# Kernel optimization log

Measured on AMD Instinct MI355X. Metric: run time of the kernel, lower is better.

Reference implementation:

```python
import jax, jax.numpy as jnp
import numpy as np

B, S, EMB, HEAD = 8, 2048, 2048, 128
ROPE_BASE = 10000.0


def _rope(x):
    # x: [B, S, D]; standard rotate-half rotary position embedding
    d = x.shape[-1]
    half = d // 2
    inv_freq = 1.0 / (ROPE_BASE ** (jnp.arange(half, dtype=jnp.float32) / half))  # [half]
    ang = jnp.arange(x.shape[-2], dtype=jnp.float32)[:, None] * inv_freq           # [S, half]
    cos, sin = jnp.cos(ang), jnp.sin(ang)
    x1, x2 = x[..., :half], x[..., half:]
    return jnp.concatenate([x1 * cos - x2 * sin, x1 * sin + x2 * cos], axis=-1)


def setup_inputs() -> dict:
    key = jax.random.key(0)
    ks = jax.random.split(key, 7)
    sc = 1.0 / np.sqrt(EMB)
    return {
        "x": jax.random.normal(ks[0], (B, S, EMB), dtype=jnp.float32),
        "Wq": jax.random.normal(ks[1], (EMB, HEAD), dtype=jnp.float32) * sc,
        "bq": jax.random.normal(ks[2], (HEAD,), dtype=jnp.float32) * 0.02,
        "Wk": jax.random.normal(ks[3], (EMB, HEAD), dtype=jnp.float32) * sc,
        "bk": jax.random.normal(ks[4], (HEAD,), dtype=jnp.float32) * 0.02,
        "Wv": jax.random.normal(ks[5], (EMB, HEAD), dtype=jnp.float32) * sc,
        "bv": jax.random.normal(ks[6], (HEAD,), dtype=jnp.float32) * 0.02,
    }


def reference(x, Wq, bq, Wk, bk, Wv, bv):
    # single-head causal self-attention with RoPE (cache=None path)
    q = _rope(x @ Wq + bq)            # [B, S, HEAD]
    k = _rope(x @ Wk + bk)            # [B, S, HEAD]
    v = x @ Wv + bv                   # [B, S, HEAD]
    scale = 1.0 / jnp.sqrt(jnp.float32(HEAD))
    scores = jnp.einsum('bqd,bkd->bqk', q, k) * scale   # [B, S, S]
    causal = jnp.tril(jnp.ones((S, S), dtype=bool))
    scores = jnp.where(causal, scores, -jnp.inf)
    weights = jax.nn.softmax(scores, axis=-1)
    return jnp.einsum('bqk,bkd->bqd', weights, v)       # [B, S, HEAD]
```

## Files before the change

kernel.cpp:

```cpp
#include <hip/hip_runtime.h>

typedef __bf16 bf16;
typedef __bf16 bf16x8 __attribute__((ext_vector_type(8)));
typedef float f32x4 __attribute__((ext_vector_type(4)));

#define S_LEN 2048
#define EMBD 2048
#define HD 128

__device__ inline void gload16(const void* g, void* l) {
  __builtin_amdgcn_global_load_lds(
      (const __attribute__((address_space(1))) unsigned int*)g,
      (__attribute__((address_space(3))) unsigned int*)l, 16, 0, 0);
}

__global__ void k_prep(const float* __restrict__ Wq, const float* __restrict__ Wk,
                       const float* __restrict__ Wv, bf16* __restrict__ wt) {
  int idx = blockIdx.x * blockDim.x + threadIdx.x;
  int k = idx & 2047;
  int n = (idx >> 11) & 127;
  int mat = idx >> 18;
  int ksrc = (k & ~63) | ((k & 63) ^ ((n & 7) << 3));
  const float* W = (mat == 0) ? Wq : ((mat == 1) ? Wk : Wv);
  wt[idx] = (bf16)W[(size_t)ksrc * HD + n];
}

__global__ __launch_bounds__(256) void k_qkv(
    const float* __restrict__ x, const bf16* __restrict__ wt,
    const float* __restrict__ bq, const float* __restrict__ bk,
    const float* __restrict__ bv, bf16* __restrict__ Qw, bf16* __restrict__ Kw,
    bf16* __restrict__ Vtw) {
  __shared__ __align__(16) bf16 xs[2][64 * 72];
  __shared__ __align__(16) bf16 wts[2][192 * 64];

  const int tid = threadIdx.x;
  const int lane = tid & 63;
  const int wn = tid >> 6;
  const int l15 = lane & 15;
  const int lh = lane >> 4;
  const int bx = blockIdx.x & 255;
  const int by = blockIdx.x >> 8;
  const int row0 = bx * 64;

  f32x4 acc[4][3];
#pragma unroll
  for (int mf = 0; mf < 4; ++mf)
#pragma unroll
    for (int f = 0; f < 3; ++f) acc[mf][f] = {};

  int xr_[4], xk_[4];
  const float* xp_[4];
#pragma unroll
  for (int i = 0; i < 4; ++i) {
    int e = (i * 256 + tid) * 4;
    xr_[i] = e >> 6;
    xk_[i] = e & 63;
    xp_[i] = x + (size_t)(row0 + xr_[i]) * EMBD + xk_[i];
  }

  const bf16* wp[6];
  int we[6];
#pragma unroll
  for (int i = 0; i < 6; ++i) {
    int e = (i * 256 + tid) * 8;
    int np = e >> 6, k = e & 63;
    int ng = (np < 128) ? by * 128 + np : 256 + by * 64 + (np - 128);
    wp[i] = wt + (size_t)ng * EMBD + k;
    we[i] = e;
  }

  auto stage_issue = [&](int ks, int buf, float4* xr) {
#pragma unroll
    for (int i = 0; i < 4; ++i) xr[i] = *(const float4*)(xp_[i] + ks * 64);
#pragma unroll
    for (int i = 0; i < 6; ++i) gload16(wp[i] + ks * 64, &wts[buf][we[i]]);
  };
  auto xwrite = [&](int buf, const float4* xr) {
#pragma unroll
    for (int i = 0; i < 4; ++i) {
      union { bf16 h[4]; uint2 u; } p;
      p.h[0] = (bf16)xr[i].x; p.h[1] = (bf16)xr[i].y;
      p.h[2] = (bf16)xr[i].z; p.h[3] = (bf16)xr[i].w;
      *(uint2*)&xs[buf][xr_[i] * 72 + xk_[i]] = p.u;
    }
  };

  {
    float4 xr[4];
    stage_issue(0, 0, xr);
    xwrite(0, xr);
  }
  __syncthreads();

  for (int ks = 0; ks < EMBD / 64; ++ks) {
    const int c = ks & 1, pbuf = c ^ 1;
    float4 xr[4];
    if (ks < EMBD / 64 - 1) stage_issue(ks + 1, pbuf, xr);

#pragma unroll
    for (int kk = 0; kk < 2; ++kk) {
      bf16x8 a[4];
#pragma unroll
      for (int mf = 0; mf < 4; ++mf)
        a[mf] = *(const bf16x8*)&xs[c][(mf * 16 + l15) * 72 + kk * 32 + lh * 8];
      const int klin = (kk * 32 + lh * 8) ^ ((l15 & 7) << 3);
#pragma unroll
      for (int f = 0; f < 3; ++f) {
        bf16x8 b = *(const bf16x8*)&wts[c][(f * 64 + wn * 16 + l15) * 64 + klin];
#pragma unroll
        for (int mf = 0; mf < 4; ++mf)
          acc[mf][f] =
              __builtin_amdgcn_mfma_f32_16x16x32_bf16(a[mf], b, acc[mf][f], 0, 0, 0);
      }
    }

    if (ks < EMBD / 64 - 1) xwrite(pbuf, xr);
    __syncthreads();
  }

  bf16* vstage = wts[0];

  {
    const int colA = by * 128 + wn * 16 + l15;
    const int colB = colA + 64;
    float biasA = (colA < 128) ? bq[colA] : bk[colA - 128];
    float biasB = (colB < 128) ? bq[colB] : bk[colB - 128];
    float invf = exp2f((float)(colA & 63) * -0.20762050593046014f);
#pragma unroll
    for (int mf = 0; mf < 4; ++mf) {
#pragma unroll
      for (int r = 0; r < 4; ++r) {
        int grow = row0 + mf * 16 + lh * 4 + r;
        int s = grow & (S_LEN - 1);
        int bb = grow >> 11;
        float xa = acc[mf][0][r] + biasA;
        float xb = acc[mf][1][r] + biasB;
        float sn, cs;
        sincosf((float)s * invf, &sn, &cs);
        float oa = xa * cs - xb * sn;
        float ob = xa * sn + xb * cs;
        if (by == 0) {
          Qw[(size_t)(bb * S_LEN + s) * HD + colA] = (bf16)oa;
          Qw[(size_t)(bb * S_LEN + s) * HD + colB] = (bf16)ob;
        } else {
          int ccA = colA - 128, ccB = colB - 128;
          int sw = (s & 7) << 3;
          Kw[(size_t)(bb * S_LEN + s) * HD + (ccA ^ sw)] = (bf16)oa;
          Kw[(size_t)(bb * S_LEN + s) * HD + (ccB ^ sw)] = (bf16)ob;
        }
      }
    }
  }
  {
    const int dvl = wn * 16 + l15;
    float biasV = bv[by * 64 + dvl];
#pragma unroll
    for (int mf = 0; mf < 4; ++mf)
#pragma unroll
      for (int r = 0; r < 4; ++r) {
        int mrow = mf * 16 + lh * 4 + r;
        vstage[dvl * 72 + mrow] = (bf16)(acc[mf][2][r] + biasV);
      }
  }
  __syncthreads();
  {
    int bb = row0 >> 11;
    int s0 = row0 & (S_LEN - 1);
#pragma unroll
    for (int i = 0; i < 2; ++i) {
      int c = i * 256 + tid;
      int dvl = c >> 3, kq = c & 7;
      uint4 v = *(const uint4*)&vstage[dvl * 72 + kq * 8];
      int dv = by * 64 + dvl;
      int slot = (kq * 8) ^ ((dvl & 7) << 3);
      *(uint4*)&Vtw[((size_t)(bb * HD + dv) << 11) + s0 + slot] = v;
    }
  }
}

__global__ __launch_bounds__(512) void k_attn(
    const bf16* __restrict__ Qw, const bf16* __restrict__ Kw,
    const bf16* __restrict__ Vtw, float* __restrict__ out) {
  __shared__ __align__(16) char arena[131072];
  __shared__ __align__(16) bf16 pld[8 * 16 * 72];
  __shared__ float mls[64], lls[64];

  bf16(*kls)[64 * 128] = (bf16(*)[64 * 128])arena;
  bf16(*vls)[128 * 64] = (bf16(*)[128 * 64])(arena + 65536);
  float* oml = (float*)arena;

  const int tid = threadIdx.x;
  const int lane = tid & 63;
  const int wave = tid >> 6;
  const int grp = wave >> 2;
  const int w4 = wave & 3;
  const int l15 = lane & 15;
  const int lh = lane >> 4;
  const int t256 = tid & 255;

  const int bid = blockIdx.x;
  const int batch = bid & 7;
  const int qt = 31 - (bid >> 3);
  const int qbase = qt * 64;
  const int nt = qt + 1;
  const int mysteps = (nt - grp + 1) >> 1;
  const int maxst = (nt + 1) >> 1;

  const bf16* kbat = Kw + (size_t)(batch * S_LEN) * HD;
  const bf16* vbat = Vtw + ((size_t)(batch * HD) << 11);

  auto stage = [&](int t, int buf) {
    bf16* kdst = kls[grp * 2 + buf];
    bf16* vdst = vls[grp * 2 + buf];
    const bf16* kbase = kbat + (size_t)(t * 64) * HD;
#pragma unroll
    for (int i = 0; i < 4; ++i) {
      int c = i * 256 + t256;
      gload16(kbase + c * 8, kdst + c * 8);
    }
    const bf16* vbase = vbat + t * 64;
#pragma unroll
    for (int i = 0; i < 4; ++i) {
      int c = i * 256 + t256;
      int dv = c >> 3, kq = (c & 7) * 8;
      gload16(vbase + ((size_t)dv << 11) + kq, vdst + c * 8);
    }
  };

  bf16x8 qa[4];
  {
    const bf16* qptr = Qw + (size_t)(batch * S_LEN + qbase + w4 * 16 + l15) * HD;
#pragma unroll
    for (int kk = 0; kk < 4; ++kk) qa[kk] = *(const bf16x8*)(qptr + kk * 32 + lh * 8);
  }

  f32x4 o[8];
#pragma unroll
  for (int i = 0; i < 8; ++i) o[i] = {};
  float m[4], lsum[4];
#pragma unroll
  for (int r = 0; r < 4; ++r) { m[r] = -__builtin_inff(); lsum[r] = 0.f; }

  const float scale = 0.08838834764831845f;

  if (mysteps > 0) stage(grp, 0);
  __syncthreads();

  for (int i = 0; i < maxst; ++i) {
    if (i + 1 < mysteps) stage(2 * (i + 1) + grp, (i + 1) & 1);
    if (i < mysteps) {
      const int t = 2 * i + grp;
      const int buf = grp * 2 + (i & 1);
      const int kv0 = t * 64;

      f32x4 sc[4];
#pragma unroll
      for (int nf = 0; nf < 4; ++nf) sc[nf] = {};
      __builtin_amdgcn_s_setprio(1);
#pragma unroll
      for (int kk = 0; kk < 4; ++kk) {
#pragma unroll
        for (int nf = 0; nf < 4; ++nf) {
          int row = nf * 16 + l15;
          int dlin = (kk * 32 + lh * 8) ^ ((row & 7) << 3);
          bf16x8 kb = *(const bf16x8*)&kls[buf][row * 128 + dlin];
          sc[nf] = __builtin_amdgcn_mfma_f32_16x16x32_bf16(qa[kk], kb, sc[nf], 0, 0, 0);
        }
      }
      __builtin_amdgcn_s_setprio(0);

      const bool diag = (t == qt);
      const int qg0 = qbase + w4 * 16 + lh * 4;
#pragma unroll
      for (int nf = 0; nf < 4; ++nf) {
        int kvg = kv0 + nf * 16 + l15;
#pragma unroll
        for (int r = 0; r < 4; ++r) {
          float v = sc[nf][r] * scale;
          if (diag && kvg > qg0 + r) v = -__builtin_inff();
          sc[nf][r] = v;
        }
      }

      float mnew[4], alpha[4], rs[4];
#pragma unroll
      for (int r = 0; r < 4; ++r) {
        float v = fmaxf(fmaxf(sc[0][r], sc[1][r]), fmaxf(sc[2][r], sc[3][r]));
#pragma unroll
        for (int sh = 1; sh < 16; sh <<= 1) v = fmaxf(v, __shfl_xor(v, sh));
        mnew[r] = fmaxf(m[r], v);
        alpha[r] = __expf(m[r] - mnew[r]);
        m[r] = mnew[r];
        rs[r] = 0.f;
      }

      bf16* pw = &pld[wave * 16 * 72];
#pragma unroll
      for (int nf = 0; nf < 4; ++nf)
#pragma unroll
        for (int r = 0; r < 4; ++r) {
          float p = __expf(sc[nf][r] - mnew[r]);
          bf16 pb = (bf16)p;
          pw[(lh * 4 + r) * 72 + nf * 16 + l15] = pb;
          rs[r] += (float)pb;
        }
#pragma unroll
      for (int r = 0; r < 4; ++r) {
        float v = rs[r];
#pragma unroll
        for (int sh = 1; sh < 16; sh <<= 1) v += __shfl_xor(v, sh);
        lsum[r] = lsum[r] * alpha[r] + v;
      }
#pragma unroll
      for (int i2 = 0; i2 < 8; ++i2)
#pragma unroll
        for (int r = 0; r < 4; ++r) o[i2][r] *= alpha[r];

      __builtin_amdgcn_s_setprio(1);
#pragma unroll
      for (int kkv = 0; kkv < 2; ++kkv) {
        bf16x8 pa = *(const bf16x8*)&pw[l15 * 72 + kkv * 32 + lh * 8];
#pragma unroll
        for (int df = 0; df < 8; ++df) {
          int dv = df * 16 + l15;
          int klin = (kkv * 32 + lh * 8) ^ ((dv & 7) << 3);
          bf16x8 vb = *(const bf16x8*)&vls[buf][dv * 64 + klin];
          o[df] = __builtin_amdgcn_mfma_f32_16x16x32_bf16(pa, vb, o[df], 0, 0, 0);
        }
      }
      __builtin_amdgcn_s_setprio(0);
    }
    __syncthreads();
  }

  if (grp == 1) {
#pragma unroll
    for (int df = 0; df < 8; ++df)
#pragma unroll
      for (int r = 0; r < 4; ++r)
        oml[(w4 * 16 + lh * 4 + r) * 128 + df * 16 + l15] = o[df][r];
    if (l15 == 0) {
#pragma unroll
      for (int r = 0; r < 4; ++r) {
        mls[w4 * 16 + lh * 4 + r] = m[r];
        lls[w4 * 16 + lh * 4 + r] = lsum[r];
      }
    }
  }
  __syncthreads();
  if (grp == 0) {
#pragma unroll
    for (int r = 0; r < 4; ++r) {
      int row = w4 * 16 + lh * 4 + r;
      float m1 = mls[row], l1 = lls[row];
      float mm = fmaxf(m[r], m1);
      float s0 = __expf(m[r] - mm);
      float s1 = __expf(m1 - mm);
      float inv = 1.0f / (lsum[r] * s0 + l1 * s1);
      float* op = out + (size_t)(batch * S_LEN + qbase + row) * HD;
#pragma unroll
      for (int df = 0; df < 8; ++df)
        op[df * 16 + l15] =
            (o[df][r] * s0 + oml[row * 128 + df * 16 + l15] * s1) * inv;
    }
  }
}

extern "C" void kernel_launch(void* const* d_in, const int* in_sizes, int n_in,
                              void* d_out, int out_size, void* d_ws, size_t ws_size,
                              hipStream_t stream) {
  const float* x = (const float*)d_in[0];
  const float* Wq = (const float*)d_in[1];
  const float* bq = (const float*)d_in[2];
  const float* Wk = (const float*)d_in[3];
  const float* bk = (const float*)d_in[4];
  const float* Wv = (const float*)d_in[5];
  const float* bv = (const float*)d_in[6];
  float* out = (float*)d_out;

  char* ws = (char*)d_ws;
  bf16* wt  = (bf16*)(ws);
  bf16* Qw  = (bf16*)(ws + (size_t)(2u << 20));
  bf16* Kw  = (bf16*)(ws + (size_t)(6u << 20));
  bf16* Vtw = (bf16*)(ws + (size_t)(10u << 20));

  hipLaunchKernelGGL(k_prep, dim3(1536), dim3(512), 0, stream, Wq, Wk, Wv, wt);
  hipLaunchKernelGGL(k_qkv, dim3(512), dim3(256), 0, stream, x, wt, bq, bk, bv,
                     Qw, Kw, Vtw);
  hipLaunchKernelGGL(k_attn, dim3(256), dim3(512), 0, stream, Qw, Kw, Vtw, out);
}
```

Measured before the change: 116.9 us.

## Retile QKV projection into three 128-column blocks and tile weight prep transpose

The QKV projection grid changes from 512 blocks covering 192 output columns each to 768 blocks covering 128 columns each (Q, K or V). It uses a 2x2 wave layout, a smaller weight LDS buffer and a 3-blocks-per-CU launch bound, and block ordering is grouped so the three column tiles of a row block are adjacent for L2 reuse of x. The weight-prep kernel becomes an LDS-tiled transpose with vectorized coalesced loads and stores, replacing the scattered per-element gather. Costs are extra reads of x across three column blocks and a more branchy epilogue.

```diff
diff --git a/kernel.cpp b/kernel.cpp
--- a/kernel.cpp
+++ b/kernel.cpp
@@ -14,39 +14,71 @@
       (__attribute__((address_space(3))) unsigned int*)l, 16, 0, 0);
 }
 
-__global__ void k_prep(const float* __restrict__ Wq, const float* __restrict__ Wk,
-                       const float* __restrict__ Wv, bf16* __restrict__ wt) {
-  int idx = blockIdx.x * blockDim.x + threadIdx.x;
-  int k = idx & 2047;
-  int n = (idx >> 11) & 127;
-  int mat = idx >> 18;
-  int ksrc = (k & ~63) | ((k & 63) ^ ((n & 7) << 3));
+__global__ __launch_bounds__(256) void k_prep(const float* __restrict__ Wq,
+                                              const float* __restrict__ Wk,
+                                              const float* __restrict__ Wv,
+                                              bf16* __restrict__ wt) {
+  __shared__ bf16 wls[64 * 72];
+
+  const int t = threadIdx.x;
+  const int bid = blockIdx.x;
+  const int mat = bid >> 6;
+  const int nt = bid & 1;
+  const int kt = (bid & 63) >> 1;
+  const int k0 = kt * 64, n0 = nt * 64;
   const float* W = (mat == 0) ? Wq : ((mat == 1) ? Wk : Wv);
-  wt[idx] = (bf16)W[(size_t)ksrc * HD + n];
+
+#pragma unroll
+  for (int i = 0; i < 4; ++i) {
+    int e = i * 256 + t;
+    int r = e >> 4, c4 = e & 15;
+    float4 v = *(const float4*)(W + (size_t)(k0 + r) * HD + n0 + c4 * 4);
+    union { bf16 h[4]; uint2 u; } p;
+    p.h[0] = (bf16)v.x; p.h[1] = (bf16)v.y;
+    p.h[2] = (bf16)v.z; p.h[3] = (bf16)v.w;
+    *(uint2*)&wls[r * 72 + c4 * 4] = p.u;
+  }
+  __syncthreads();
+#pragma unroll
+  for (int i = 0; i < 2; ++i) {
+    int slot = i * 256 + t;
+    int n_loc = slot >> 3, kq = slot & 7;
+    int n = n0 + n_loc;
+    int kbase = (kq * 8) ^ ((n & 7) << 3);
+    union { bf16 h[8]; uint4 u; } p;
+#pragma unroll
+    for (int j = 0; j < 8; ++j) p.h[j] = wls[(kbase + j) * 72 + n_loc];
+    *(uint4*)&wt[(size_t)(mat * HD + n) * EMBD + k0 + kq * 8] = p.u;
+  }
 }
 
-__global__ __launch_bounds__(256) void k_qkv(
+__global__ __launch_bounds__(256, 3) void k_qkv(
     const float* __restrict__ x, const bf16* __restrict__ wt,
     const float* __restrict__ bq, const float* __restrict__ bk,
     const float* __restrict__ bv, bf16* __restrict__ Qw, bf16* __restrict__ Kw,
     bf16* __restrict__ Vtw) {
   __shared__ __align__(16) bf16 xs[2][64 * 72];
-  __shared__ __align__(16) bf16 wts[2][192 * 64];
+  __shared__ __align__(16) bf16 wts[2][128 * 64];
 
   const int tid = threadIdx.x;
   const int lane = tid & 63;
-  const int wn = tid >> 6;
+  const int wave = tid >> 6;
+  const int wm = wave >> 1;
+  const int wn = wave & 1;
   const int l15 = lane & 15;
   const int lh = lane >> 4;
-  const int bx = blockIdx.x & 255;
-  const int by = blockIdx.x >> 8;
-  const int row0 = bx * 64;
-
-  f32x4 acc[4][3];
-#pragma unroll
-  for (int mf = 0; mf < 4; ++mf)
-#pragma unroll
-    for (int f = 0; f < 3; ++f) acc[mf][f] = {};
+
+  const int bid = blockIdx.x;
+  const int g = bid >> 3;
+  const int by = g % 3;
+  const int mt = (bid & 7) + 8 * (g / 3);
+  const int row0 = mt * 64;
+
+  f32x4 acc[2][4];
+#pragma unroll
+  for (int mf = 0; mf < 2; ++mf)
+#pragma unroll
+    for (int f = 0; f < 4; ++f) acc[mf][f] = {};
 
   int xr_[4], xk_[4];
   const float* xp_[4];
@@ -57,23 +89,21 @@
     xk_[i] = e & 63;
     xp_[i] = x + (size_t)(row0 + xr_[i]) * EMBD + xk_[i];
   }
-
-  const bf16* wp[6];
-  int we[6];
-#pragma unroll
-  for (int i = 0; i < 6; ++i) {
+  const bf16* wp_[4];
+  int we_[4];
+#pragma unroll
+  for (int i = 0; i < 4; ++i) {
     int e = (i * 256 + tid) * 8;
     int np = e >> 6, k = e & 63;
-    int ng = (np < 128) ? by * 128 + np : 256 + by * 64 + (np - 128);
-    wp[i] = wt + (size_t)ng * EMBD + k;
-    we[i] = e;
+    wp_[i] = wt + (size_t)(by * 128 + np) * EMBD + k;
+    we_[i] = e;
   }
 
   auto stage_issue = [&](int ks, int buf, float4* xr) {
 #pragma unroll
     for (int i = 0; i < 4; ++i) xr[i] = *(const float4*)(xp_[i] + ks * 64);
 #pragma unroll
-    for (int i = 0; i < 6; ++i) gload16(wp[i] + ks * 64, &wts[buf][we[i]]);
+    for (int i = 0; i < 4; ++i) gload16(wp_[i] + ks * 64, &wts[buf][we_[i]]);
   };
   auto xwrite = [&](int buf, const float4* xr) {
 #pragma unroll
@@ -99,16 +129,17 @@
 
 #pragma unroll
     for (int kk = 0; kk < 2; ++kk) {
-      bf16x8 a[4];
-#pragma unroll
-      for (int mf = 0; mf < 4; ++mf)
-        a[mf] = *(const bf16x8*)&xs[c][(mf * 16 + l15) * 72 + kk * 32 + lh * 8];
-      const int klin = (kk * 32 + lh * 8) ^ ((l15 & 7) << 3);
-#pragma unroll
-      for (int f = 0; f < 3; ++f) {
-        bf16x8 b = *(const bf16x8*)&wts[c][(f * 64 + wn * 16 + l15) * 64 + klin];
-#pragma unroll
-        for (int mf = 0; mf < 4; ++mf)
+      bf16x8 a[2];
+#pragma unroll
+      for (int mf = 0; mf < 2; ++mf)
+        a[mf] = *(const bf16x8*)&xs[c][(wm * 32 + mf * 16 + l15) * 72 + kk * 32 + lh * 8];
+#pragma unroll
+      for (int f = 0; f < 4; ++f) {
+        int col = (f & 1) * 16 + (f >> 1) * 64 + wn * 32 + l15;
+        int klin = (kk * 32 + lh * 8) ^ ((col & 7) << 3);
+        bf16x8 b = *(const bf16x8*)&wts[c][col * 64 + klin];
+#pragma unroll
+        for (int mf = 0; mf < 2; ++mf)
           acc[mf][f] =
               __builtin_amdgcn_mfma_f32_16x16x32_bf16(a[mf], b, acc[mf][f], 0, 0, 0);
       }
@@ -118,61 +149,61 @@
     __syncthreads();
   }
 
-  bf16* vstage = wts[0];
-
-  {
-    const int colA = by * 128 + wn * 16 + l15;
-    const int colB = colA + 64;
-    float biasA = (colA < 128) ? bq[colA] : bk[colA - 128];
-    float biasB = (colB < 128) ? bq[colB] : bk[colB - 128];
-    float invf = exp2f((float)(colA & 63) * -0.20762050593046014f);
-#pragma unroll
-    for (int mf = 0; mf < 4; ++mf) {
-#pragma unroll
-      for (int r = 0; r < 4; ++r) {
-        int grow = row0 + mf * 16 + lh * 4 + r;
-        int s = grow & (S_LEN - 1);
-        int bb = grow >> 11;
-        float xa = acc[mf][0][r] + biasA;
-        float xb = acc[mf][1][r] + biasB;
-        float sn, cs;
-        sincosf((float)s * invf, &sn, &cs);
-        float oa = xa * cs - xb * sn;
-        float ob = xa * sn + xb * cs;
-        if (by == 0) {
-          Qw[(size_t)(bb * S_LEN + s) * HD + colA] = (bf16)oa;
-          Qw[(size_t)(bb * S_LEN + s) * HD + colB] = (bf16)ob;
-        } else {
-          int ccA = colA - 128, ccB = colB - 128;
-          int sw = (s & 7) << 3;
-          Kw[(size_t)(bb * S_LEN + s) * HD + (ccA ^ sw)] = (bf16)oa;
-          Kw[(size_t)(bb * S_LEN + s) * HD + (ccB ^ sw)] = (bf16)ob;
-        }
-      }
-    }
-  }
-  {
-    const int dvl = wn * 16 + l15;
-    float biasV = bv[by * 64 + dvl];
-#pragma unroll
-    for (int mf = 0; mf < 4; ++mf)
-#pragma unroll
-      for (int r = 0; r < 4; ++r) {
-        int mrow = mf * 16 + lh * 4 + r;
-        vstage[dvl * 72 + mrow] = (bf16)(acc[mf][2][r] + biasV);
-      }
-  }
-  __syncthreads();
-  {
-    int bb = row0 >> 11;
-    int s0 = row0 & (S_LEN - 1);
-#pragma unroll
-    for (int i = 0; i < 2; ++i) {
+  const int bb = row0 >> 11;
+  const int s0 = row0 & (S_LEN - 1);
+
+  if (by < 2) {
+    const float* bias = (by == 0) ? bq : bk;
+#pragma unroll
+    for (int fp = 0; fp < 2; ++fp) {
+      const int colA = wn * 32 + fp * 16 + l15;
+      const int colB = colA + 64;
+      float biasA = bias[colA], biasB = bias[colB];
+      float invf = exp2f((float)colA * -0.20762050593046014f);
+#pragma unroll
+      for (int mf = 0; mf < 2; ++mf) {
+#pragma unroll
+        for (int r = 0; r < 4; ++r) {
+          int s = s0 + wm * 32 + mf * 16 + lh * 4 + r;
+          float xa = acc[mf][fp][r] + biasA;
+          float xb = acc[mf][fp + 2][r] + biasB;
+          float sn, cs;
+          sincosf((float)s * invf, &sn, &cs);
+          float oa = xa * cs - xb * sn;
+          float ob = xa * sn + xb * cs;
+          if (by == 0) {
+            Qw[(size_t)(bb * S_LEN + s) * HD + colA] = (bf16)oa;
+            Qw[(size_t)(bb * S_LEN + s) * HD + colB] = (bf16)ob;
+          } else {
+            int sw = (s & 7) << 3;
+            Kw[(size_t)(bb * S_LEN + s) * HD + (colA ^ sw)] = (bf16)oa;
+            Kw[(size_t)(bb * S_LEN + s) * HD + (colB ^ sw)] = (bf16)ob;
+          }
+        }
+      }
+    }
+  } else {
+    __syncthreads();
+    bf16* vstage = &xs[0][0];
+#pragma unroll
+    for (int f = 0; f < 4; ++f) {
+      int dv = (f & 1) * 16 + (f >> 1) * 64 + wn * 32 + l15;
+      float biasV = bv[dv];
+#pragma unroll
+      for (int mf = 0; mf < 2; ++mf)
+#pragma unroll
+        for (int r = 0; r < 4; ++r) {
+          int mrow = wm * 32 + mf * 16 + lh * 4 + r;
+          vstage[dv * 72 + mrow] = (bf16)(acc[mf][f][r] + biasV);
+        }
+    }
+    __syncthreads();
+#pragma unroll
+    for (int i = 0; i < 4; ++i) {
       int c = i * 256 + tid;
-      int dvl = c >> 3, kq = c & 7;
-      uint4 v = *(const uint4*)&vstage[dvl * 72 + kq * 8];
-      int dv = by * 64 + dvl;
-      int slot = (kq * 8) ^ ((dvl & 7) << 3);
+      int dv = c >> 3, kq = c & 7;
+      uint4 v = *(const uint4*)&vstage[dv * 72 + kq * 8];
+      int slot = (kq * 8) ^ ((dv & 7) << 3);
       *(uint4*)&Vtw[((size_t)(bb * HD + dv) << 11) + s0 + slot] = v;
     }
   }
@@ -384,8 +415,8 @@
   bf16* Kw  = (bf16*)(ws + (size_t)(6u << 20));
   bf16* Vtw = (bf16*)(ws + (size_t)(10u << 20));
 
-  hipLaunchKernelGGL(k_prep, dim3(1536), dim3(512), 0, stream, Wq, Wk, Wv, wt);
-  hipLaunchKernelGGL(k_qkv, dim3(512), dim3(256), 0, stream, x, wt, bq, bk, bv,
+  hipLaunchKernelGGL(k_prep, dim3(192), dim3(256), 0, stream, Wq, Wk, Wv, wt);
+  hipLaunchKernelGGL(k_qkv, dim3(768), dim3(256), 0, stream, x, wt, bq, bk, bv,
                      Qw, Kw, Vtw);
   hipLaunchKernelGGL(k_attn, dim3(256), dim3(512), 0, stream, Qw, Kw, Vtw, out);
 }
```

Measured after the change: 102.6 us. 1.14x faster.
